# Kernel optimization log

Measured on AMD Instinct MI355X. Metric: run time of the kernel, lower is better.

## Reference

```python
import jax, jax.numpy as jnp
import numpy as np

N, D = 2048, 1024
H, KV, HD = 16, 4, 64
REPEATS = H // KV
SCALE = HD ** -0.5


def setup_inputs() -> dict:
    key = jax.random.key(0)
    ks = jax.random.split(key, 6)
    x = jax.random.normal(ks[0], (N, D), dtype=jnp.float32)
    # rotary tables: cos/sin of interleaved-pair angles (llama-style view_as_complex)
    pos = jnp.arange(N, dtype=jnp.float32)[:, None]
    inv_freq = 1.0 / (10000.0 ** (jnp.arange(0, HD, 2, dtype=jnp.float32) / HD))
    ang = pos * inv_freq[None, :]  # (N, HD//2)
    freqs_cos = jnp.cos(ang)
    freqs_sin = jnp.sin(ang)
    s = 0.02
    Wq = jax.random.normal(ks[1], (D, H * HD), dtype=jnp.float32) * s
    Wk = jax.random.normal(ks[2], (D, KV * HD), dtype=jnp.float32) * s
    Wv = jax.random.normal(ks[3], (D, KV * HD), dtype=jnp.float32) * s
    Wo = jax.random.normal(ks[4], (H * HD, D), dtype=jnp.float32) * s
    return {"x": x, "freqs_cos": freqs_cos, "freqs_sin": freqs_sin,
            "Wq": Wq, "Wk": Wk, "Wv": Wv, "Wo": Wo}


def _rope(t, cos, sin):
    # t: (N, heads, HD); interleaved complex pairs (even=real, odd=imag)
    tr = t[..., 0::2]
    ti = t[..., 1::2]
    c = cos[:, None, :]
    s = sin[:, None, :]
    out_r = tr * c - ti * s
    out_i = tr * s + ti * c
    return jnp.stack([out_r, out_i], axis=-1).reshape(t.shape)


def reference(x, freqs_cos, freqs_sin, Wq, Wk, Wv, Wo):
    n = x.shape[0]
    xq = (x @ Wq).reshape(n, H, HD)
    xk = (x @ Wk).reshape(n, KV, HD)
    xv = (x @ Wv).reshape(n, KV, HD)
    xq = _rope(xq, freqs_cos, freqs_sin)
    xk = _rope(xk, freqs_cos, freqs_sin)
    # repeat_kv along head dim (GQA)
    k = jnp.repeat(xk, REPEATS, axis=1)  # (n, H, HD)
    v = jnp.repeat(xv, REPEATS, axis=1)
    # memory_efficient_attention with mask=None: full attention over token axis
    scores = jnp.einsum('nhd,mhd->hnm', xq, k) * SCALE
    attn = jax.nn.softmax(scores, axis=-1)
    out = jnp.einsum('hnm,mhd->nhd', attn, v)
    return out.reshape(n, H * HD) @ Wo
```

## Files before the change

### kernel.cpp

```cpp
#include <hip/hip_runtime.h>

#define N_TOK 2048
#define DMODEL 1024
#define NH 16
#define NKV 4
#define HDIM 64
#define SCALE_LOG2E 0.1803368801111204f

typedef __attribute__((ext_vector_type(8))) short short8;
typedef __attribute__((ext_vector_type(4))) float f32x4;
typedef __attribute__((ext_vector_type(16))) float f32x16;
typedef unsigned short u16;
typedef unsigned int u32;

__device__ __forceinline__ u16 f2bf(float x) {
    u32 u = __float_as_uint(x);
    u += 0x7FFF + ((u >> 16) & 1);
    return (u16)(u >> 16);
}
__device__ __forceinline__ u32 pack2(float a, float b) {
    return (u32)f2bf(a) | ((u32)f2bf(b) << 16);
}
__device__ __forceinline__ u32 pack2t(float a, float b) {
    return __builtin_amdgcn_perm(__float_as_uint(b), __float_as_uint(a), 0x07060302u);
}

__global__ __launch_bounds__(256) void prep(
    const float* __restrict__ Wq, const float* __restrict__ Wk,
    const float* __restrict__ Wv, const float* __restrict__ Wo,
    const float* __restrict__ x,
    u16* __restrict__ Wqt, u16* __restrict__ Wkt, u16* __restrict__ Wvt,
    u16* __restrict__ Wot, u16* __restrict__ xb)
{
    const int z = blockIdx.z;
    const int t = threadIdx.x;
    if (z == 4) {
        size_t base = ((size_t)(blockIdx.y * 16 + blockIdx.x)) * 8192;
#pragma unroll
        for (int i = 0; i < 8; ++i) {
            float4 v = *(const float4*)(x + base + i * 1024 + t * 4);
            uint2 p; p.x = pack2(v.x, v.y); p.y = pack2(v.z, v.w);
            *(uint2*)(xb + base + i * 1024 + t * 4) = p;
        }
        return;
    }
    const float* W; u16* Wt; int NC;
    if      (z == 0) { W = Wq; Wt = Wqt; NC = 1024; }
    else if (z == 1) { W = Wk; Wt = Wkt; NC = 256; }
    else if (z == 2) { W = Wv; Wt = Wvt; NC = 256; }
    else             { W = Wo; Wt = Wot; NC = 1024; }
    const int n0 = blockIdx.x * 64;
    if (n0 >= NC) return;
    const int k0 = blockIdx.y * 64;
    __shared__ float T[64][68];
    const int row = t >> 2, cs = (t & 3) * 16;
#pragma unroll
    for (int i = 0; i < 4; ++i)
        *(float4*)&T[row][cs + i * 4] =
            *(const float4*)(W + (size_t)(k0 + row) * NC + n0 + cs + i * 4);
    __syncthreads();
    const int nl = t >> 2, ks = (t & 3) * 16;
    u32 pk[8];
#pragma unroll
    for (int i = 0; i < 8; ++i)
        pk[i] = pack2(T[ks + 2 * i][nl], T[ks + 2 * i + 1][nl]);
    u16* dst = Wt + (size_t)(n0 + nl) * DMODEL + k0 + ks;
    uint4 w0; w0.x = pk[0]; w0.y = pk[1]; w0.z = pk[2]; w0.w = pk[3];
    uint4 w1; w1.x = pk[4]; w1.y = pk[5]; w1.z = pk[6]; w1.w = pk[7];
    *(uint4*)(dst) = w0;
    *(uint4*)(dst + 8) = w1;
}

__global__ __launch_bounds__(256, 2) void gemm_qkv(
    const u16* __restrict__ A,
    const u16* __restrict__ B0, const u16* __restrict__ B1, const u16* __restrict__ B2,
    u16* __restrict__ D0, u16* __restrict__ D1, u16* __restrict__ FVout,
    const float* __restrict__ fc, const float* __restrict__ fs)
{
    __shared__ u16 As[2][128][72];
    __shared__ u16 Bs[2][64][72];
    const int t = threadIdx.x;
    const int m0 = blockIdx.x * 128;
    const int by = blockIdx.y;

    const u16* Bt; int nl0, ep;
    u16* dbf = nullptr; int dstride = 0; float epsc = 1.f;
    if (by < 16)      { Bt = B0; nl0 = by * 64;        dbf = D0; ep = 1; dstride = 1024;
                        epsc = SCALE_LOG2E; }
    else if (by < 20) { Bt = B1; nl0 = (by - 16) * 64; dbf = D1; ep = 1; dstride = 256; }
    else              { Bt = B2; nl0 = (by - 20) * 64; ep = 2; }

    const int w = t >> 6, lane = t & 63;
    const int quad = lane >> 4, l15 = lane & 15;
    const int wm = (w >> 1) * 64, wn = (w & 1) * 32;
    const int arow = t >> 1, ac = (t & 1) * 32;
    const int brow = t >> 2, bc = (t & 3) * 16;

    const u16* Ap = A + (size_t)(m0 + arow) * DMODEL + ac;
    const u16* Bp = Bt + (size_t)(nl0 + brow) * DMODEL + bc;

    f32x4 acc[4][2];
#pragma unroll
    for (int i = 0; i < 4; ++i)
#pragma unroll
        for (int j = 0; j < 2; ++j) acc[i][j] = {0.f, 0.f, 0.f, 0.f};

    uint4 a_r[4], b_r[2];
#pragma unroll
    for (int ci = 0; ci < 4; ++ci) a_r[ci] = *(const uint4*)(Ap + ci * 8);
    b_r[0] = *(const uint4*)(Bp);
    b_r[1] = *(const uint4*)(Bp + 8);
#pragma unroll
    for (int ci = 0; ci < 4; ++ci) *(uint4*)&As[0][arow][ac + ci * 8] = a_r[ci];
    *(uint4*)&Bs[0][brow][bc]     = b_r[0];
    *(uint4*)&Bs[0][brow][bc + 8] = b_r[1];
    __syncthreads();

    for (int it = 0; it < 16; ++it) {
        const int cur = it & 1;
        const bool more = (it + 1) < 16;
        if (more) {
            const int k1 = (it + 1) * 64;
#pragma unroll
            for (int ci = 0; ci < 4; ++ci) a_r[ci] = *(const uint4*)(Ap + k1 + ci * 8);
            b_r[0] = *(const uint4*)(Bp + k1);
            b_r[1] = *(const uint4*)(Bp + k1 + 8);
        }
#pragma unroll
        for (int c = 0; c < 2; ++c) {
            short8 af[4], bf[2];
#pragma unroll
            for (int i = 0; i < 4; ++i)
                af[i] = *(const short8*)&As[cur][wm + i * 16 + l15][c * 32 + quad * 8];
#pragma unroll
            for (int j = 0; j < 2; ++j)
                bf[j] = *(const short8*)&Bs[cur][wn + j * 16 + l15][c * 32 + quad * 8];
#pragma unroll
            for (int i = 0; i < 4; ++i)
#pragma unroll
                for (int j = 0; j < 2; ++j)
                    acc[i][j] = __builtin_amdgcn_mfma_f32_16x16x32_bf16(af[i], bf[j], acc[i][j], 0, 0, 0);
        }
        if (more) {
            const int nx = cur ^ 1;
#pragma unroll
            for (int ci = 0; ci < 4; ++ci) *(uint4*)&As[nx][arow][ac + ci * 8] = a_r[ci];
            *(uint4*)&Bs[nx][brow][bc]     = b_r[0];
            *(uint4*)&Bs[nx][brow][bc + 8] = b_r[1];
            __syncthreads();
        }
    }

#pragma unroll
    for (int i = 0; i < 4; ++i)
#pragma unroll
        for (int j = 0; j < 2; ++j) {
            const int cl = nl0 + wn + j * 16 + l15;
            if (ep == 1) {
#pragma unroll
                for (int r4 = 0; r4 < 4; ++r4) {
                    const int r = m0 + wm + i * 16 + quad * 4 + r4;
                    float own = acc[i][j][r4];
                    float other = __shfl_xor(own, 1, 64);
                    const int p = (cl & 63) >> 1;
                    const float c = fc[r * 32 + p] * epsc, s = fs[r * 32 + p] * epsc;
                    float outv = ((cl & 1) == 0) ? (own * c - other * s)
                                                 : (other * s + own * c);
                    dbf[(size_t)r * dstride + cl] = f2bf(outv);
                }
            } else {
                const int rb = m0 + wm + i * 16 + quad * 4;
                const int g = cl >> 6, d = cl & 63;
                const int d2 = d >> 5, dl = d & 31;
                const int keyblk = rb >> 7, kg = (rb >> 5) & 3;
                const int kst = (rb >> 4) & 1, hb = (rb >> 3) & 1, jv = rb & 7;
                size_t idx = ((((((size_t)(g * 16 + keyblk) * 4 + kg) * 2 + kst) * 2 + d2)
                               * 2 + hb) * 32 + dl) * 8 + jv;
                uint2 pk;
                pk.x = pack2(acc[i][j][0], acc[i][j][1]);
                pk.y = pack2(acc[i][j][2], acc[i][j][3]);
                *(uint2*)(FVout + idx) = pk;
            }
        }
}

__global__ __launch_bounds__(256, 2) void gemm_out(
    const u16* __restrict__ A, const u16* __restrict__ Bt, float* __restrict__ Dout)
{
    __shared__ u16 As[2][64][72];
    __shared__ u16 Bs[2][64][72];
    const int t = threadIdx.x;
    const int m0 = blockIdx.x * 64;
    const int nl0 = blockIdx.y * 64;

    const int w = t >> 6, lane = t & 63;
    const int quad = lane >> 4, l15 = lane & 15;
    const int wm = (w >> 1) * 32, wn = (w & 1) * 32;
    const int srow = t >> 2, sk = (t & 3) * 16;

    const u16* Ap = A + (size_t)(m0 + srow) * DMODEL + sk;
    const u16* Bp = Bt + (size_t)(nl0 + srow) * DMODEL + sk;

    f32x4 acc[2][2];
#pragma unroll
    for (int i = 0; i < 2; ++i)
#pragma unroll
        for (int j = 0; j < 2; ++j) acc[i][j] = {0.f, 0.f, 0.f, 0.f};

    uint4 a_r[2], b_r[2];
    a_r[0] = *(const uint4*)(Ap);     a_r[1] = *(const uint4*)(Ap + 8);
    b_r[0] = *(const uint4*)(Bp);     b_r[1] = *(const uint4*)(Bp + 8);
    *(uint4*)&As[0][srow][sk]     = a_r[0];
    *(uint4*)&As[0][srow][sk + 8] = a_r[1];
    *(uint4*)&Bs[0][srow][sk]     = b_r[0];
    *(uint4*)&Bs[0][srow][sk + 8] = b_r[1];
    __syncthreads();

    for (int it = 0; it < 16; ++it) {
        const int cur = it & 1;
        const bool more = (it + 1) < 16;
        if (more) {
            const int k1 = (it + 1) * 64;
            a_r[0] = *(const uint4*)(Ap + k1);     a_r[1] = *(const uint4*)(Ap + k1 + 8);
            b_r[0] = *(const uint4*)(Bp + k1);     b_r[1] = *(const uint4*)(Bp + k1 + 8);
        }
#pragma unroll
        for (int c = 0; c < 2; ++c) {
            short8 af[2], bf[2];
#pragma unroll
            for (int i = 0; i < 2; ++i)
                af[i] = *(const short8*)&As[cur][wm + i * 16 + l15][c * 32 + quad * 8];
#pragma unroll
            for (int j = 0; j < 2; ++j)
                bf[j] = *(const short8*)&Bs[cur][wn + j * 16 + l15][c * 32 + quad * 8];
#pragma unroll
            for (int i = 0; i < 2; ++i)
#pragma unroll
                for (int j = 0; j < 2; ++j)
                    acc[i][j] = __builtin_amdgcn_mfma_f32_16x16x32_bf16(af[i], bf[j], acc[i][j], 0, 0, 0);
        }
        if (more) {
            const int nx = cur ^ 1;
            *(uint4*)&As[nx][srow][sk]     = a_r[0];
            *(uint4*)&As[nx][srow][sk + 8] = a_r[1];
            *(uint4*)&Bs[nx][srow][sk]     = b_r[0];
            *(uint4*)&Bs[nx][srow][sk + 8] = b_r[1];
            __syncthreads();
        }
    }

#pragma unroll
    for (int i = 0; i < 2; ++i)
#pragma unroll
        for (int j = 0; j < 2; ++j) {
            const int cl = nl0 + wn + j * 16 + l15;
#pragma unroll
            for (int r4 = 0; r4 < 4; ++r4) {
                const int r = m0 + wm + i * 16 + quad * 4 + r4;
                Dout[(size_t)r * 1024 + cl] = acc[i][j][r4];
            }
        }
}

__global__ __launch_bounds__(256, 2) void attn_part(
    const u16* __restrict__ Qb, const u16* __restrict__ Kb,
    const u16* __restrict__ FV, float* __restrict__ Opart, float* __restrict__ Lpart)
{
    __shared__ u16 Ks[2][128][72];
    __shared__ u16 Ps[4][32][40];

    const int t = threadIdx.x;
    const int n0 = blockIdx.x * 128;
    const int h = blockIdx.y, kvh = h >> 2;
    const int ksp = blockIdx.z;
    const int w = t >> 6, lane = t & 63;
    const int hi = lane >> 5, l31 = lane & 31;
    const int srow = t >> 1, ssel = (t & 1) * 32;

    const u16* qp = Qb + (size_t)(n0 + w * 32 + l31) * (NH * HDIM) + h * HDIM + hi * 8;
    short8 qf[4];
#pragma unroll
    for (int s = 0; s < 4; ++s) qf[s] = *(const short8*)(qp + s * 16);

    const u16* kbase = Kb + (size_t)(ksp * 1024 + srow) * (NKV * HDIM) + kvh * HDIM + ssel;
    const u16* fvb = FV + ((size_t)kvh * 16 * 8192) + (size_t)lane * 8;

    f32x16 o[2];
#pragma unroll
    for (int d2 = 0; d2 < 2; ++d2)
#pragma unroll
        for (int r = 0; r < 16; ++r) o[d2][r] = 0.f;
    float l_acc = 0.f;

#pragma unroll
    for (int c = 0; c < 4; ++c)
        *(uint4*)&Ks[0][srow][ssel + c * 8] = *(const uint4*)(kbase + c * 8);
    __syncthreads();

    for (int rd = 0; rd < 8; ++rd) {
        const int cur = rd & 1, nxt = cur ^ 1;
        const int rdn = (rd + 1) & 7;
        uint4 kr[4];
#pragma unroll
        for (int c = 0; c < 4; ++c)
            kr[c] = *(const uint4*)(kbase + (size_t)(rdn * 128) * (NKV * HDIM) + c * 8);
        const int keyblk = ksp * 8 + rd;

#pragma unroll
        for (int kg = 0; kg < 4; ++kg) {
            short8 vf[2][2];
#pragma unroll
            for (int s = 0; s < 2; ++s)
#pragma unroll
                for (int d2 = 0; d2 < 2; ++d2)
                    vf[s][d2] = *(const short8*)(fvb +
                        ((((size_t)keyblk * 4 + kg) * 2 + s) * 2 + d2) * 512);
            f32x16 sa;
#pragma unroll
            for (int r = 0; r < 16; ++r) sa[r] = 0.f;
#pragma unroll
            for (int s = 0; s < 4; ++s) {
                short8 kf = *(const short8*)&Ks[cur][kg * 32 + l31][s * 16 + hi * 8];
                sa = __builtin_amdgcn_mfma_f32_32x32x16_bf16(kf, qf[s], sa, 0, 0, 0);
            }
            float p[16];
#pragma unroll
            for (int r = 0; r < 16; ++r) p[r] = __builtin_amdgcn_exp2f(sa[r]);
            l_acc += ((p[0] + p[1]) + (p[2] + p[3])) + ((p[4] + p[5]) + (p[6] + p[7]))
                   + ((p[8] + p[9]) + (p[10] + p[11])) + ((p[12] + p[13]) + (p[14] + p[15]));
#pragma unroll
            for (int blk = 0; blk < 4; ++blk) {
                uint2 pk;
                pk.x = pack2t(p[blk * 4 + 0], p[blk * 4 + 1]);
                pk.y = pack2t(p[blk * 4 + 2], p[blk * 4 + 3]);
                *(uint2*)&Ps[w][l31][blk * 8 + 4 * hi] = pk;
            }
            const short8 ap0 = *(const short8*)&Ps[w][l31][hi * 8];
            const short8 ap1 = *(const short8*)&Ps[w][l31][16 + hi * 8];
#pragma unroll
            for (int d2 = 0; d2 < 2; ++d2) {
                o[d2] = __builtin_amdgcn_mfma_f32_32x32x16_bf16(ap0, vf[0][d2], o[d2], 0, 0, 0);
                o[d2] = __builtin_amdgcn_mfma_f32_32x32x16_bf16(ap1, vf[1][d2], o[d2], 0, 0, 0);
            }
        }
#pragma unroll
        for (int c = 0; c < 4; ++c)
            *(uint4*)&Ks[nxt][srow][ssel + c * 8] = kr[c];
        __syncthreads();
    }

    l_acc += __shfl_xor(l_acc, 32, 64);
    if (lane < 32)
        Lpart[(size_t)ksp * (NH * N_TOK) + h * N_TOK + n0 + w * 32 + lane] = l_acc;
    float* op = Opart + (size_t)ksp * N_TOK * 1024;
#pragma unroll
    for (int d2 = 0; d2 < 2; ++d2)
#pragma unroll
        for (int r = 0; r < 16; ++r) {
            const int q = n0 + w * 32 + (r & 3) + 8 * (r >> 2) + 4 * hi;
            op[(size_t)q * 1024 + h * HDIM + d2 * 32 + l31] = o[d2][r];
        }
}

__global__ __launch_bounds__(256) void combine(
    const float* __restrict__ Opart, const float* __restrict__ Lpart,
    u16* __restrict__ aob)
{
    const int row = blockIdx.x, t = threadIdx.x;
    const int h = t >> 4;
    const float4 a = *(const float4*)(Opart + (size_t)row * 1024 + t * 4);
    const float4 b = *(const float4*)(Opart + (size_t)N_TOK * 1024 + (size_t)row * 1024 + t * 4);
    const float li = 1.f / (Lpart[h * N_TOK + row] + Lpart[NH * N_TOK + h * N_TOK + row]);
    uint2 ov;
    ov.x = pack2((a.x + b.x) * li, (a.y + b.y) * li);
    ov.y = pack2((a.z + b.z) * li, (a.w + b.w) * li);
    *(uint2*)(aob + (size_t)row * 1024 + t * 4) = ov;
}

extern "C" void kernel_launch(void* const* d_in, const int* in_sizes, int n_in,
                              void* d_out, int out_size, void* d_ws, size_t ws_size,
                              hipStream_t stream) {
    const float* x  = (const float*)d_in[0];
    const float* fc = (const float*)d_in[1];
    const float* fs = (const float*)d_in[2];
    const float* Wq = (const float*)d_in[3];
    const float* Wk = (const float*)d_in[4];
    const float* Wv = (const float*)d_in[5];
    const float* Wo = (const float*)d_in[6];
    float* out = (float*)d_out;

    u16* ws  = (u16*)d_ws;
    u16* xb  = ws;
    u16* Wqt = xb  + (size_t)2048 * 1024;
    u16* Wkt = Wqt + (size_t)1024 * 1024;
    u16* Wvt = Wkt + (size_t)256 * 1024;
    u16* Wot = Wvt + (size_t)256 * 1024;
    u16* qb  = Wot + (size_t)1024 * 1024;
    u16* kb  = qb  + (size_t)2048 * 1024;
    u16* fv  = kb  + (size_t)2048 * 256;
    u16* aob = fv  + (size_t)256 * 2048;
    float* opart = (float*)(aob + (size_t)2048 * 1024);
    float* lpart = opart + (size_t)2 * 2048 * 1024;

    prep<<<dim3(16, 16, 5), dim3(256), 0, stream>>>(Wq, Wk, Wv, Wo, x,
                                                    Wqt, Wkt, Wvt, Wot, xb);
    gemm_qkv<<<dim3(16, 24), dim3(256), 0, stream>>>(xb, Wqt, Wkt, Wvt,
                                                     qb, kb, fv, fc, fs);
    attn_part<<<dim3(16, 16, 2), dim3(256), 0, stream>>>(qb, kb, fv, opart, lpart);
    combine<<<dim3(2048), dim3(256), 0, stream>>>(opart, lpart, aob);
    gemm_out<<<dim3(32, 16), dim3(256), 0, stream>>>(aob, Wot, out);
}
```

Measured before the change: 136.8 us.

## Fuse split-K attention combine into block via intra-block key halves

Replaces the two-way split over the key axis across blocks, which wrote fp32 partial outputs and row sums to global memory for a separate combine kernel, with an in-block split. Two wave pairs each handle half the keys for 64 queries, then reduce through shared memory and write bf16 output directly. Row sums are now computed with an extra MFMA against a ones vector instead of scalar adds. This drops a kernel launch and the fp32 partial round trip, but each block now stalls on a final barrier and reduction and runs extra MFMAs.

New measurement: 137.2 us. No clear change (+0.3%).

```diff
diff --git a/kernel.cpp b/kernel.cpp
--- a/kernel.cpp
+++ b/kernel.cpp
@@ -262,72 +262,76 @@
         }
 }
 
-__global__ __launch_bounds__(256, 2) void attn_part(
+__global__ __launch_bounds__(256, 2) void attn(
     const u16* __restrict__ Qb, const u16* __restrict__ Kb,
-    const u16* __restrict__ FV, float* __restrict__ Opart, float* __restrict__ Lpart)
+    const u16* __restrict__ FV, u16* __restrict__ Ob)
 {
-    __shared__ u16 Ks[2][128][72];
+    __shared__ u16 Ks[2][2][64][72];
     __shared__ u16 Ps[4][32][40];
 
     const int t = threadIdx.x;
-    const int n0 = blockIdx.x * 128;
+    const int n0 = blockIdx.x * 64;
     const int h = blockIdx.y, kvh = h >> 2;
-    const int ksp = blockIdx.z;
     const int w = t >> 6, lane = t & 63;
     const int hi = lane >> 5, l31 = lane & 31;
+    const int qgrp = w & 1, khalf = w >> 1;
     const int srow = t >> 1, ssel = (t & 1) * 32;
-
-    const u16* qp = Qb + (size_t)(n0 + w * 32 + l31) * (NH * HDIM) + h * HDIM + hi * 8;
+    const int khalf_s = srow >> 6, klocal = srow & 63;
+
+    const short8 ones = {(short)0x3F80, (short)0x3F80, (short)0x3F80, (short)0x3F80,
+                         (short)0x3F80, (short)0x3F80, (short)0x3F80, (short)0x3F80};
+
+    const u16* qp = Qb + (size_t)(n0 + qgrp * 32 + l31) * (NH * HDIM) + h * HDIM + hi * 8;
     short8 qf[4];
 #pragma unroll
     for (int s = 0; s < 4; ++s) qf[s] = *(const short8*)(qp + s * 16);
 
-    const u16* kbase = Kb + (size_t)(ksp * 1024 + srow) * (NKV * HDIM) + kvh * HDIM + ssel;
+    const u16* kbase = Kb + (size_t)(khalf_s * 1024 + klocal) * (NKV * HDIM) + kvh * HDIM + ssel;
     const u16* fvb = FV + ((size_t)kvh * 16 * 8192) + (size_t)lane * 8;
 
-    f32x16 o[2];
+    f32x16 o[2], o_l;
 #pragma unroll
     for (int d2 = 0; d2 < 2; ++d2)
 #pragma unroll
         for (int r = 0; r < 16; ++r) o[d2][r] = 0.f;
-    float l_acc = 0.f;
+#pragma unroll
+    for (int r = 0; r < 16; ++r) o_l[r] = 0.f;
 
 #pragma unroll
     for (int c = 0; c < 4; ++c)
-        *(uint4*)&Ks[0][srow][ssel + c * 8] = *(const uint4*)(kbase + c * 8);
+        *(uint4*)&Ks[0][khalf_s][klocal][ssel + c * 8] = *(const uint4*)(kbase + c * 8);
     __syncthreads();
 
-    for (int rd = 0; rd < 8; ++rd) {
+    for (int rd = 0; rd < 16; ++rd) {
         const int cur = rd & 1, nxt = cur ^ 1;
-        const int rdn = (rd + 1) & 7;
+        const int rdn = (rd + 1) & 15;
         uint4 kr[4];
 #pragma unroll
         for (int c = 0; c < 4; ++c)
-            kr[c] = *(const uint4*)(kbase + (size_t)(rdn * 128) * (NKV * HDIM) + c * 8);
-        const int keyblk = ksp * 8 + rd;
-
-#pragma unroll
-        for (int kg = 0; kg < 4; ++kg) {
+            kr[c] = *(const uint4*)(kbase + (size_t)(rdn * 64) * (NKV * HDIM) + c * 8);
+
+#pragma unroll
+        for (int kg = 0; kg < 2; ++kg) {
+            const int kg_global = khalf * 32 + rd * 2 + kg;
+            const int keyblk = kg_global >> 2, kgi = kg_global & 3;
             short8 vf[2][2];
 #pragma unroll
             for (int s = 0; s < 2; ++s)
 #pragma unroll
                 for (int d2 = 0; d2 < 2; ++d2)
                     vf[s][d2] = *(const short8*)(fvb +
-                        ((((size_t)keyblk * 4 + kg) * 2 + s) * 2 + d2) * 512);
+                        ((((size_t)keyblk * 4 + kgi) * 2 + s) * 2 + d2) * 512);
             f32x16 sa;
 #pragma unroll
             for (int r = 0; r < 16; ++r) sa[r] = 0.f;
 #pragma unroll
             for (int s = 0; s < 4; ++s) {
-                short8 kf = *(const short8*)&Ks[cur][kg * 32 + l31][s * 16 + hi * 8];
+                short8 kf = *(const short8*)&Ks[cur][khalf][kg * 32 + l31][s * 16 + hi * 8];
                 sa = __builtin_amdgcn_mfma_f32_32x32x16_bf16(kf, qf[s], sa, 0, 0, 0);
             }
             float p[16];
 #pragma unroll
             for (int r = 0; r < 16; ++r) p[r] = __builtin_amdgcn_exp2f(sa[r]);
-            l_acc += ((p[0] + p[1]) + (p[2] + p[3])) + ((p[4] + p[5]) + (p[6] + p[7]))
-                   + ((p[8] + p[9]) + (p[10] + p[11])) + ((p[12] + p[13]) + (p[14] + p[15]));
 #pragma unroll
             for (int blk = 0; blk < 4; ++blk) {
                 uint2 pk;
@@ -342,39 +346,50 @@
                 o[d2] = __builtin_amdgcn_mfma_f32_32x32x16_bf16(ap0, vf[0][d2], o[d2], 0, 0, 0);
                 o[d2] = __builtin_amdgcn_mfma_f32_32x32x16_bf16(ap1, vf[1][d2], o[d2], 0, 0, 0);
             }
+            o_l = __builtin_amdgcn_mfma_f32_32x32x16_bf16(ap0, ones, o_l, 0, 0, 0);
+            o_l = __builtin_amdgcn_mfma_f32_32x32x16_bf16(ap1, ones, o_l, 0, 0, 0);
         }
 #pragma unroll
         for (int c = 0; c < 4; ++c)
-            *(uint4*)&Ks[nxt][srow][ssel + c * 8] = kr[c];
+            *(uint4*)&Ks[nxt][khalf_s][klocal][ssel + c * 8] = kr[c];
         __syncthreads();
     }
 
-    l_acc += __shfl_xor(l_acc, 32, 64);
-    if (lane < 32)
-        Lpart[(size_t)ksp * (NH * N_TOK) + h * N_TOK + n0 + w * 32 + lane] = l_acc;
-    float* op = Opart + (size_t)ksp * N_TOK * 1024;
-#pragma unroll
-    for (int d2 = 0; d2 < 2; ++d2)
+    float* Xf = (float*)&Ks[0][0][0][0];
+    if (khalf == 1) {
+#pragma unroll
+        for (int d2 = 0; d2 < 2; ++d2)
+#pragma unroll
+            for (int r = 0; r < 16; ++r) {
+                const int q32 = (r & 3) + 8 * (r >> 2) + 4 * hi;
+                Xf[qgrp * 2048 + q32 * 64 + d2 * 32 + l31] = o[d2][r];
+            }
+        if (l31 == 0) {
+#pragma unroll
+            for (int r = 0; r < 16; ++r) {
+                const int q32 = (r & 3) + 8 * (r >> 2) + 4 * hi;
+                Xf[4096 + qgrp * 32 + q32] = o_l[r];
+            }
+        }
+    }
+    __syncthreads();
+    if (khalf == 0) {
+        float linv[16];
 #pragma unroll
         for (int r = 0; r < 16; ++r) {
-            const int q = n0 + w * 32 + (r & 3) + 8 * (r >> 2) + 4 * hi;
-            op[(size_t)q * 1024 + h * HDIM + d2 * 32 + l31] = o[d2][r];
-        }
-}
-
-__global__ __launch_bounds__(256) void combine(
-    const float* __restrict__ Opart, const float* __restrict__ Lpart,
-    u16* __restrict__ aob)
-{
-    const int row = blockIdx.x, t = threadIdx.x;
-    const int h = t >> 4;
-    const float4 a = *(const float4*)(Opart + (size_t)row * 1024 + t * 4);
-    const float4 b = *(const float4*)(Opart + (size_t)N_TOK * 1024 + (size_t)row * 1024 + t * 4);
-    const float li = 1.f / (Lpart[h * N_TOK + row] + Lpart[NH * N_TOK + h * N_TOK + row]);
-    uint2 ov;
-    ov.x = pack2((a.x + b.x) * li, (a.y + b.y) * li);
-    ov.y = pack2((a.z + b.z) * li, (a.w + b.w) * li);
-    *(uint2*)(aob + (size_t)row * 1024 + t * 4) = ov;
+            const int q32 = (r & 3) + 8 * (r >> 2) + 4 * hi;
+            linv[r] = 1.f / (o_l[r] + Xf[4096 + qgrp * 32 + q32]);
+        }
+#pragma unroll
+        for (int d2 = 0; d2 < 2; ++d2)
+#pragma unroll
+            for (int r = 0; r < 16; ++r) {
+                const int q32 = (r & 3) + 8 * (r >> 2) + 4 * hi;
+                const float val = o[d2][r] + Xf[qgrp * 2048 + q32 * 64 + d2 * 32 + l31];
+                const int qrow = n0 + qgrp * 32 + q32;
+                Ob[(size_t)qrow * (NH * HDIM) + h * HDIM + d2 * 32 + l31] = f2bf(val * linv[r]);
+            }
+    }
 }
 
 extern "C" void kernel_launch(void* const* d_in, const int* in_sizes, int n_in,
@@ -399,14 +414,11 @@
     u16* kb  = qb  + (size_t)2048 * 1024;
     u16* fv  = kb  + (size_t)2048 * 256;
     u16* aob = fv  + (size_t)256 * 2048;
-    float* opart = (float*)(aob + (size_t)2048 * 1024);
-    float* lpart = opart + (size_t)2 * 2048 * 1024;
 
     prep<<<dim3(16, 16, 5), dim3(256), 0, stream>>>(Wq, Wk, Wv, Wo, x,
                                                     Wqt, Wkt, Wvt, Wot, xb);
     gemm_qkv<<<dim3(16, 24), dim3(256), 0, stream>>>(xb, Wqt, Wkt, Wvt,
                                                      qb, kb, fv, fc, fs);
-    attn_part<<<dim3(16, 16, 2), dim3(256), 0, stream>>>(qb, kb, fv, opart, lpart);
-    combine<<<dim3(2048), dim3(256), 0, stream>>>(opart, lpart, aob);
+    attn<<<dim3(32, 16), dim3(256), 0, stream>>>(qb, kb, fv, aob);
     gemm_out<<<dim3(32, 16), dim3(256), 0, stream>>>(aob, Wot, out);
 }
```
